# Optimization experiments

Hardware: AMD Instinct MI355X
Metric: run time of the kernel (lower is better)

Reference implementation:

```python
import jax, jax.numpy as jnp
import numpy as np

EMBED = 1024
HEADS = 16
HEAD_DIM = EMBED // HEADS
SCALING = HEAD_DIM ** -0.5
R = 16
LORA_SCALE = 32.0 / R  # alpha / r
NEG = jnp.finfo(jnp.float32).min


def lora_linear(x, W, A, B):
    # y = x @ W.T + (x @ A.T) @ B.T * scale   (LinearLora, bias=False)
    return x @ W.T + ((x @ A.T) @ B.T) * LORA_SCALE


def setup_inputs() -> dict:
    key = jax.random.key(0)
    ks = jax.random.split(key, 14)
    B, T, D = 1, 4096, EMBED
    hidden_states = jax.random.normal(ks[0], (B, T, D), jnp.float32)
    # causal additive mask (bsz, 1, tgt, src): 0 on/below diag, dtype-min above
    i = jnp.arange(T)
    causal = jnp.where(i[:, None] >= i[None, :], 0.0, NEG).astype(jnp.float32)
    attention_mask = jnp.broadcast_to(causal, (B, 1, T, T))
    s = 0.02
    def w(k, shape):
        return jax.random.normal(k, shape, jnp.float32) * s
    return dict(
        hidden_states=hidden_states,
        attention_mask=attention_mask,
        Wq=w(ks[1], (D, D)), Wk=w(ks[2], (D, D)), Wv=w(ks[3], (D, D)), Wo=w(ks[4], (D, D)),
        Aq=w(ks[5], (R, D)), Bq=jnp.zeros((D, R), jnp.float32) + w(ks[6], (D, R)),
        Ak=w(ks[7], (R, D)), Bk=w(ks[8], (D, R)),
        Av=w(ks[9], (R, D)), Bv=w(ks[10], (D, R)),
        Ao=w(ks[11], (R, D)), Bo=w(ks[12], (D, R)),
    )


def reference(hidden_states, attention_mask, Wq, Wk, Wv, Wo,
              Aq, Bq, Ak, Bk, Av, Bv, Ao, Bo):
    bsz, tgt_len, _ = hidden_states.shape
    H, Hd = HEADS, HEAD_DIM

    q = lora_linear(hidden_states, Wq, Aq, Bq) * SCALING
    k = lora_linear(hidden_states, Wk, Ak, Bk)
    v = lora_linear(hidden_states, Wv, Av, Bv)

    # (b, t, H, Hd)
    q = q.reshape(bsz, tgt_len, H, Hd)
    k = k.reshape(bsz, tgt_len, H, Hd)
    v = v.reshape(bsz, tgt_len, H, Hd)

    # scores (b, H, t, s)
    attn = jnp.einsum('bthd,bshd->bhts', q, k)
    attn = attn + attention_mask
    attn = jnp.maximum(attn, NEG)
    attn = jax.nn.softmax(attn, axis=-1)  # dropout p=0 / eval mode

    out = jnp.einsum('bhts,bshd->bthd', attn, v)
    out = out.reshape(bsz, tgt_len, H * Hd)
    out = lora_linear(out, Wo, Ao, Bo)
    return out
```

## Files before the change

kernel.cpp:

```cpp
#include <hip/hip_runtime.h>
#include <cmath>
#include <cstdint>

typedef unsigned short u16;
typedef __attribute__((ext_vector_type(8))) __bf16 bf16x8;
typedef __attribute__((ext_vector_type(4))) __bf16 bf16x4;
typedef __attribute__((ext_vector_type(4))) short s16x4;
typedef __attribute__((ext_vector_type(4))) float f32x4;

__device__ __forceinline__ u16 f2bf(float f) {
    union { float f; unsigned u; } v; v.f = f;
    unsigned r = v.u + 0x7fffu + ((v.u >> 16) & 1u);
    return (u16)(r >> 16);
}

__device__ __forceinline__ void gload_lds(const u16* g, u16* l) {
    __builtin_amdgcn_global_load_lds((__attribute__((address_space(1))) void*)g,
                                     (__attribute__((address_space(3))) void*)l,
                                     16, 0, 0);
}

__device__ __forceinline__ f32x4 mfma16(s16x4 a, s16x4 b, f32x4 c) {
#if __has_builtin(__builtin_amdgcn_mfma_f32_16x16x16bf16_1k)
    return __builtin_amdgcn_mfma_f32_16x16x16bf16_1k(a, b, c, 0, 0, 0);
#else
    asm("v_mfma_f32_16x16x16_bf16 %0, %1, %2, %3"
        : "=v"(c) : "v"(a), "v"(b), "0"(c));
    return c;
#endif
}

__global__ __launch_bounds__(256) void prep_all(
        const float* __restrict__ X,
        const float* __restrict__ Wq, const float* __restrict__ Wk,
        const float* __restrict__ Wv, const float* __restrict__ Wo,
        const float* __restrict__ Aq, const float* __restrict__ Bq,
        const float* __restrict__ Ak, const float* __restrict__ Bk,
        const float* __restrict__ Av, const float* __restrict__ Bv,
        const float* __restrict__ Ao, const float* __restrict__ Bo,
        u16* __restrict__ Wqkv, u16* __restrict__ Wob, u16* __restrict__ Xb) {
    const int p = blockIdx.y;
    const int idx = blockIdx.x * 256 + threadIdx.x;
    if (p == 4) {
        float4 v = ((const float4*)X)[idx];
        ushort4 o;
        o.x = f2bf(v.x); o.y = f2bf(v.y); o.z = f2bf(v.z); o.w = f2bf(v.w);
        ((ushort4*)Xb)[idx] = o;
        return;
    }
    const int n = idx >> 10, d = idx & 1023;
    const float* W; const float* A; const float* B;
    switch (p) {
        case 0: W = Wq; A = Aq; B = Bq; break;
        case 1: W = Wk; A = Ak; B = Bk; break;
        case 2: W = Wv; A = Av; B = Bv; break;
        default: W = Wo; A = Ao; B = Bo; break;
    }
    float lora = 0.f;
#pragma unroll
    for (int r = 0; r < 16; r++) lora += B[n * 16 + r] * A[r * 1024 + d];
    float v = W[idx] + 2.0f * lora;
    if (p == 0) v *= 0.125f * 1.44269504088896340736f;
    if (p < 3) Wqkv[(size_t)p * 1048576 + idx] = f2bf(v);
    else       Wob[idx] = f2bf(v);
}

template <bool F32OUT>
__global__ __launch_bounds__(256, 3) void gemm_bt(const u16* __restrict__ A,
                                                  const u16* __restrict__ B,
                                                  void* __restrict__ C, int ldc) {
    __shared__ __align__(16) u16 As[128 * 64];
    __shared__ __align__(16) u16 Bs[128 * 64];
    const int tid = threadIdx.x;
    const int lane = tid & 63, wave = tid >> 6;
    const int quad = lane >> 4, l16 = lane & 15;
    const int wm = (wave >> 1) * 64, wn = (wave & 1) * 64;
    const size_t m0 = (size_t)blockIdx.y * 128, n0 = (size_t)blockIdx.x * 128;
    const u16* Ap = A + m0 * 1024;
    const u16* Bp = B + n0 * 1024;
    const int xsw = l16 & 7;
    f32x4 acc[4][4] = {};
    for (int k0 = 0; k0 < 1024; k0 += 64) {
#pragma unroll
        for (int hh = 0; hh < 4; hh++) {
            int c = tid + hh * 256;
            int row = c >> 3, cg = (c & 7) ^ (row & 7);
            gload_lds(Ap + (size_t)row * 1024 + k0 + cg * 8, As + c * 8);
            gload_lds(Bp + (size_t)row * 1024 + k0 + cg * 8, Bs + c * 8);
        }
        asm volatile("s_waitcnt vmcnt(0)" ::: "memory");
        __syncthreads();
#pragma unroll
        for (int kf = 0; kf < 2; kf++) {
            bf16x8 af[4], bfr[4];
#pragma unroll
            for (int i = 0; i < 4; i++) {
                af[i]  = *(const bf16x8*)(As + (wm + i * 16 + l16) * 64
                                             + ((kf * 4 + quad) ^ xsw) * 8);
                bfr[i] = *(const bf16x8*)(Bs + (wn + i * 16 + l16) * 64
                                             + ((kf * 4 + quad) ^ xsw) * 8);
            }
#pragma unroll
            for (int mi = 0; mi < 4; mi++)
#pragma unroll
                for (int ni = 0; ni < 4; ni++)
                    acc[mi][ni] = __builtin_amdgcn_mfma_f32_16x16x32_bf16(
                            af[mi], bfr[ni], acc[mi][ni], 0, 0, 0);
        }
        __syncthreads();
    }
#pragma unroll
    for (int mi = 0; mi < 4; mi++)
#pragma unroll
        for (int ni = 0; ni < 4; ni++)
#pragma unroll
            for (int r = 0; r < 4; r++) {
                size_t row = m0 + wm + mi * 16 + quad * 4 + r;
                size_t col = n0 + wn + ni * 16 + l16;
                if (F32OUT) ((float*)C)[row * ldc + col] = acc[mi][ni][r];
                else        ((u16*)C)[row * ldc + col] = f2bf(acc[mi][ni][r]);
            }
}

template <bool F32OUT>
__global__ __launch_bounds__(256, 3) void gemm_bt64(const u16* __restrict__ A,
                                                    const u16* __restrict__ B,
                                                    void* __restrict__ C, int ldc) {
    __shared__ __align__(16) u16 As[64 * 64];
    __shared__ __align__(16) u16 Bs[128 * 64];
    const int tid = threadIdx.x;
    const int lane = tid & 63, wave = tid >> 6;
    const int quad = lane >> 4, l16 = lane & 15;
    const int wm = (wave >> 1) * 32, wn = (wave & 1) * 64;
    const size_t m0 = (size_t)blockIdx.y * 64, n0 = (size_t)blockIdx.x * 128;
    const u16* Ap = A + m0 * 1024;
    const u16* Bp = B + n0 * 1024;
    const int xsw = l16 & 7;
    f32x4 acc[2][4] = {};
    for (int k0 = 0; k0 < 1024; k0 += 64) {
#pragma unroll
        for (int hh = 0; hh < 2; hh++) {
            int c = tid + hh * 256;
            int row = c >> 3, cg = (c & 7) ^ (row & 7);
            gload_lds(Ap + (size_t)row * 1024 + k0 + cg * 8, As + c * 8);
        }
#pragma unroll
        for (int hh = 0; hh < 4; hh++) {
            int c = tid + hh * 256;
            int row = c >> 3, cg = (c & 7) ^ (row & 7);
            gload_lds(Bp + (size_t)row * 1024 + k0 + cg * 8, Bs + c * 8);
        }
        asm volatile("s_waitcnt vmcnt(0)" ::: "memory");
        __syncthreads();
#pragma unroll
        for (int kf = 0; kf < 2; kf++) {
            bf16x8 af[2], bfr[4];
#pragma unroll
            for (int i = 0; i < 2; i++)
                af[i] = *(const bf16x8*)(As + (wm + i * 16 + l16) * 64
                                            + ((kf * 4 + quad) ^ xsw) * 8);
#pragma unroll
            for (int i = 0; i < 4; i++)
                bfr[i] = *(const bf16x8*)(Bs + (wn + i * 16 + l16) * 64
                                             + ((kf * 4 + quad) ^ xsw) * 8);
#pragma unroll
            for (int mi = 0; mi < 2; mi++)
#pragma unroll
                for (int ni = 0; ni < 4; ni++)
                    acc[mi][ni] = __builtin_amdgcn_mfma_f32_16x16x32_bf16(
                            af[mi], bfr[ni], acc[mi][ni], 0, 0, 0);
        }
        __syncthreads();
    }
#pragma unroll
    for (int mi = 0; mi < 2; mi++)
#pragma unroll
        for (int ni = 0; ni < 4; ni++)
#pragma unroll
            for (int r = 0; r < 4; r++) {
                size_t row = m0 + wm + mi * 16 + quad * 4 + r;
                size_t col = n0 + wn + ni * 16 + l16;
                if (F32OUT) ((float*)C)[row * ldc + col] = acc[mi][ni][r];
                else        ((u16*)C)[row * ldc + col] = f2bf(acc[mi][ni][r]);
            }
}

__global__ __launch_bounds__(256) void transpose_v(const u16* __restrict__ Y,
                                                   u16* __restrict__ Vt) {
    __shared__ u16 tile[64][68];
    const int dv0 = blockIdx.x * 64;
    const int t0  = blockIdx.y * 64;
    const int tid = threadIdx.x;
#pragma unroll
    for (int p = 0; p < 4; p++) {
        int pos = tid + p * 256;
        int row = pos >> 4;
        int c4  = (pos & 15) * 4;
        ushort4 v = *(const ushort4*)(Y + (size_t)(t0 + row) * 3072 + 2048 + dv0 + c4);
        tile[row][c4 + 0] = v.x; tile[row][c4 + 1] = v.y;
        tile[row][c4 + 2] = v.z; tile[row][c4 + 3] = v.w;
    }
    __syncthreads();
#pragma unroll
    for (int p = 0; p < 4; p++) {
        int pos = tid + p * 256;
        int orow = pos >> 4;
        int oc4  = (pos & 15) * 4;
        ushort4 o;
        o.x = tile[oc4 + 0][orow]; o.y = tile[oc4 + 1][orow];
        o.z = tile[oc4 + 2][orow]; o.w = tile[oc4 + 3][orow];
        *(ushort4*)(Vt + (size_t)(dv0 + orow) * 4096 + t0 + oc4) = o;
    }
}

__device__ const unsigned char SCHED[48] = {
    (1<<6)|31, (0<<6)|15, (1<<6)|30, (2<<6)|30, (2<<6)|29, (0<<6)|14, (2<<6)|28, (1<<6)|27,
    (2<<6)|27, (0<<6)|13, (2<<6)|26, (2<<6)|25, (0<<6)|12, (1<<6)|24, (2<<6)|24, (2<<6)|23,
    (2<<6)|31, (1<<6)|29, (1<<6)|28, (1<<6)|26, (1<<6)|25, (1<<6)|23, (1<<6)|22, (1<<6)|21,
    (1<<6)|20, (2<<6)|20, (1<<6)|19, (2<<6)|19, (2<<6)|21, (2<<6)|22, (0<<6)|10, (0<<6)|11,
    (0<<6)|0,  (0<<6)|1,  (0<<6)|2,  (0<<6)|3,  (0<<6)|4,  (0<<6)|5,  (0<<6)|6,  (0<<6)|7,
    (1<<6)|16, (2<<6)|16, (1<<6)|18, (0<<6)|9,  (1<<6)|17, (2<<6)|17, (2<<6)|18, (0<<6)|8
};

__global__ __launch_bounds__(256, 3) void flash_attn(
        const u16* __restrict__ Y,
        const u16* __restrict__ Vt,
        u16* __restrict__ O,
        float* __restrict__ OpA,
        float* __restrict__ OpB,
        float* __restrict__ lA,
        float* __restrict__ lB) {
    __shared__ __align__(16) u16 lds[16384];
    const int tid = threadIdx.x;
    const int wave = tid >> 6, lane = tid & 63;
    const int quad = lane >> 4, l16 = lane & 15;
    const int bid = blockIdx.x;
    const int g = bid >> 4, h = bid & 15;
    const int sc = SCHED[g];
    const int p = sc & 63, mode = sc >> 6;
    const int t0 = (mode == 2) ? p + 1 : 0;
    const int t1 = (mode == 1) ? p + 1 : 2 * p + 2;
    const int q0w = p * 128 + wave * 32;
    const u16* Kbase = Y + 1024 + h * 64;
    const u16* Vbase = Vt + (size_t)(h * 64) * 4096;
    const int xsw = l16 & 7;

    bf16x8 qf[2][2];
#pragma unroll
    for (int qh = 0; qh < 2; qh++)
#pragma unroll
        for (int kf = 0; kf < 2; kf++)
            qf[qh][kf] = *(const bf16x8*)(Y + (size_t)(q0w + qh * 16 + l16) * 3072
                                            + h * 64 + kf * 32 + quad * 8);

    f32x4 oaccT[2][4] = {};
    f32x4 lacc[2] = {};
    const s16x4 ones = { (short)0x3F80, (short)0x3F80,
                         (short)0x3F80, (short)0x3F80 };

    {
        const int s0p = t0 * 64;
        u16* Kn = lds + (t0 & 1) * 8192;
#pragma unroll
        for (int pp = 0; pp < 2; pp++) {
            int c = pp * 256 + tid;
            int row = c >> 3, cg = (c & 7) ^ (row & 7);
            gload_lds(Kbase + (size_t)(s0p + row) * 3072 + cg * 8, Kn + c * 8);
            gload_lds(Vbase + (size_t)row * 4096 + s0p + cg * 8, Kn + 4096 + c * 8);
        }
    }

#pragma unroll 1
    for (int t = t0; t < t1; t++) {
        const int s0 = t * 64;
        u16* Ks = lds + (t & 1) * 8192;
        u16* Vs = Ks + 4096;
        asm volatile("s_waitcnt vmcnt(0)" ::: "memory");
        __syncthreads();

        if (t + 1 < t1) {
            u16* Kn = lds + ((t + 1) & 1) * 8192;
            const int sn = s0 + 64;
#pragma unroll
            for (int pp = 0; pp < 2; pp++) {
                int c = pp * 256 + tid;
                int row = c >> 3, cg = (c & 7) ^ (row & 7);
                gload_lds(Kbase + (size_t)(sn + row) * 3072 + cg * 8, Kn + c * 8);
                gload_lds(Vbase + (size_t)row * 4096 + sn + cg * 8, Kn + 4096 + c * 8);
            }
        }

        bf16x8 kfr[4][2];
#pragma unroll
        for (int ni = 0; ni < 4; ni++) {
            int row = ni * 16 + l16;
            kfr[ni][0] = *(const bf16x8*)(Ks + row * 64 + ((quad) ^ xsw) * 8);
            kfr[ni][1] = *(const bf16x8*)(Ks + row * 64 + ((4 + quad) ^ xsw) * 8);
        }
        s16x4 vfr[4][4];
#pragma unroll
        for (int nj = 0; nj < 4; nj++) {
            int row = nj * 16 + l16;
#pragma unroll
            for (int ni = 0; ni < 4; ni++) {
                int cc = ni * 2 + (quad >> 1);
                vfr[nj][ni] = *(const s16x4*)(Vs + row * 64 + (cc ^ xsw) * 8
                                                 + (quad & 1) * 4);
            }
        }

        const bool diag = (t >= 2 * p);
#pragma unroll
        for (int qh = 0; qh < 2; qh++) {
            f32x4 sacc[4] = {};
#pragma unroll
            for (int ni = 0; ni < 4; ni++) {
                sacc[ni] = __builtin_amdgcn_mfma_f32_16x16x32_bf16(
                        kfr[ni][0], qf[qh][0], sacc[ni], 0, 0, 0);
                sacc[ni] = __builtin_amdgcn_mfma_f32_16x16x32_bf16(
                        kfr[ni][1], qf[qh][1], sacc[ni], 0, 0, 0);
            }
            const int qg = q0w + qh * 16 + l16;
#pragma unroll
            for (int ni = 0; ni < 4; ni++) {
                if (diag) {
#pragma unroll
                    for (int r = 0; r < 4; r++) {
                        int sg = s0 + ni * 16 + quad * 4 + r;
                        if (sg > qg) sacc[ni][r] = -INFINITY;
                    }
                }
                f32x4 pe;
#pragma unroll
                for (int r = 0; r < 4; r++)
                    pe[r] = __builtin_amdgcn_exp2f(sacc[ni][r]);
                bf16x4 tt = { (__bf16)pe[0], (__bf16)pe[1],
                              (__bf16)pe[2], (__bf16)pe[3] };
                s16x4 pf = __builtin_bit_cast(s16x4, tt);
                lacc[qh] = mfma16(ones, pf, lacc[qh]);
#pragma unroll
                for (int nj = 0; nj < 4; nj++)
                    oaccT[qh][nj] = mfma16(vfr[nj][ni], pf, oaccT[qh][nj]);
            }
        }
    }

    __syncthreads();
    if (mode == 0) {
        u16* scr = lds + wave * 1152;
#pragma unroll
        for (int qh = 0; qh < 2; qh++) {
            float inv = 1.0f / lacc[qh][0];
#pragma unroll
            for (int nj = 0; nj < 4; nj++) {
                bf16x4 t4 = { (__bf16)(oaccT[qh][nj][0] * inv),
                              (__bf16)(oaccT[qh][nj][1] * inv),
                              (__bf16)(oaccT[qh][nj][2] * inv),
                              (__bf16)(oaccT[qh][nj][3] * inv) };
                *(s16x4*)(scr + l16 * 72 + nj * 16 + quad * 4) =
                        __builtin_bit_cast(s16x4, t4);
            }
            asm volatile("s_waitcnt lgkmcnt(0)" ::: "memory");
#pragma unroll
            for (int pp = 0; pp < 2; pp++) {
                int row = pp * 8 + (lane >> 3);
                int seg = (lane & 7) * 8;
                bf16x8 d = *(const bf16x8*)(scr + row * 72 + seg);
                *(bf16x8*)(O + (size_t)(q0w + qh * 16 + row) * 1024 + h * 64 + seg) = d;
            }
            asm volatile("s_waitcnt lgkmcnt(0)" ::: "memory");
        }
    } else {
        float* Op = (mode == 1) ? OpA : OpB;
        float* lp = (mode == 1) ? lA : lB;
        float* scr = (float*)lds + wave * 1088;
#pragma unroll
        for (int qh = 0; qh < 2; qh++) {
#pragma unroll
            for (int nj = 0; nj < 4; nj++)
                *(f32x4*)(scr + l16 * 68 + nj * 16 + quad * 4) = oaccT[qh][nj];
            asm volatile("s_waitcnt lgkmcnt(0)" ::: "memory");
#pragma unroll
            for (int it = 0; it < 4; it++) {
                int row = (lane >> 4) + it * 4;
                int seg = (lane & 15) * 4;
                f32x4 d = *(const f32x4*)(scr + row * 68 + seg);
                *(f32x4*)(Op + (size_t)(q0w + qh * 16 + row - 2048) * 1024
                             + h * 64 + seg) = d;
            }
            if (lane < 16)
                lp[(size_t)(q0w + qh * 16 + lane - 2048) * 16 + h] = lacc[qh][0];
            asm volatile("s_waitcnt lgkmcnt(0)" ::: "memory");
        }
    }
}

__global__ __launch_bounds__(256) void combine_o(
        const float* __restrict__ OpA, const float* __restrict__ OpB,
        const float* __restrict__ lA, const float* __restrict__ lB,
        u16* __restrict__ O) {
    const int idx = blockIdx.x * 256 + threadIdx.x;
    const int r = idx >> 7;
    const int c8 = (idx & 127) * 8;
    const int h = c8 >> 6;
    const float inv = 1.0f / (lA[r * 16 + h] + lB[r * 16 + h]);
    const float* a = OpA + (size_t)r * 1024 + c8;
    const float* b = OpB + (size_t)r * 1024 + c8;
    float4 a0 = *(const float4*)a, a1 = *(const float4*)(a + 4);
    float4 b0 = *(const float4*)b, b1 = *(const float4*)(b + 4);
    ushort4 o0, o1;
    o0.x = f2bf((a0.x + b0.x) * inv); o0.y = f2bf((a0.y + b0.y) * inv);
    o0.z = f2bf((a0.z + b0.z) * inv); o0.w = f2bf((a0.w + b0.w) * inv);
    o1.x = f2bf((a1.x + b1.x) * inv); o1.y = f2bf((a1.y + b1.y) * inv);
    o1.z = f2bf((a1.z + b1.z) * inv); o1.w = f2bf((a1.w + b1.w) * inv);
    u16* op = O + (size_t)(2048 + r) * 1024 + c8;
    *(ushort4*)op = o0;
    *(ushort4*)(op + 4) = o1;
}


extern "C" void kernel_launch(void* const* d_in, const int* in_sizes, int n_in,
                              void* d_out, int out_size, void* d_ws, size_t ws_size,
                              hipStream_t stream) {
    const float* X  = (const float*)d_in[0];
    const float* Wq = (const float*)d_in[2];
    const float* Wk = (const float*)d_in[3];
    const float* Wv = (const float*)d_in[4];
    const float* Wo = (const float*)d_in[5];
    const float* Aq = (const float*)d_in[6];
    const float* Bq = (const float*)d_in[7];
    const float* Ak = (const float*)d_in[8];
    const float* Bk = (const float*)d_in[9];
    const float* Av = (const float*)d_in[10];
    const float* Bv = (const float*)d_in[11];
    const float* Ao = (const float*)d_in[12];
    const float* Bo = (const float*)d_in[13];

    char* ws = (char*)d_ws;
    u16*   Xb   = (u16*)(ws);
    float* OpA  = (float*)(ws);
    u16*   Wqkv = (u16*)(ws + (8u  << 20));
    float* OpB  = (float*)(ws + (8u  << 20));
    u16*   Y    = (u16*)(ws + (16u << 20));
    u16*   Vt   = (u16*)(ws + (40u << 20));
    u16*   Ob   = (u16*)(ws + (48u << 20));
    u16*   Wob  = (u16*)(ws + (56u << 20));
    float* lA   = (float*)(ws + (58u << 20));
    float* lB   = (float*)(ws + (58u << 20) + (128u << 10));

    prep_all<<<dim3(4096, 5), 256, 0, stream>>>(X, Wq, Wk, Wv, Wo, Aq, Bq, Ak, Bk,
                                                Av, Bv, Ao, Bo, Wqkv, Wob, Xb);
    gemm_bt<false><<<dim3(24, 32), 256, 0, stream>>>(Xb, Wqkv, Y, 3072);
    transpose_v<<<dim3(16, 64), 256, 0, stream>>>(Y, Vt);
    flash_attn<<<dim3(768), 256, 0, stream>>>(Y, Vt, Ob, OpA, OpB, lA, lB);
    combine_o<<<dim3(1024), 256, 0, stream>>>(OpA, OpB, lA, lB, Ob);
    gemm_bt64<true><<<dim3(8, 64), 256, 0, stream>>>(Ob, Wob, d_out, 1024);
}
```

Measured before the change: 259.4 us.

## Load K/V fragments directly from global memory instead of staging through LDS

Removes the double-buffered LDS staging of K and V tiles (global_load_lds plus barriers) and has each wave load its K and V MFMA fragments straight from global memory through per-row pointers. It also shrinks the shared allocation to just the epilogue scratch space. This drops the per-iteration __syncthreads and the LDS traffic, but each of the four waves now fetches the same K/V data on its own, with no prefetch of the next tile to hide latency.

```diff
diff --git a/kernel.cpp b/kernel.cpp
--- a/kernel.cpp
+++ b/kernel.cpp
@@ -230,7 +230,7 @@
         float* __restrict__ OpB,
         float* __restrict__ lA,
         float* __restrict__ lB) {
-    __shared__ __align__(16) u16 lds[16384];
+    __shared__ __align__(16) u16 lds[8704];
     const int tid = threadIdx.x;
     const int wave = tid >> 6, lane = tid & 63;
     const int quad = lane >> 4, l16 = lane & 15;
@@ -241,9 +241,6 @@
     const int t0 = (mode == 2) ? p + 1 : 0;
     const int t1 = (mode == 1) ? p + 1 : 2 * p + 2;
     const int q0w = p * 128 + wave * 32;
-    const u16* Kbase = Y + 1024 + h * 64;
-    const u16* Vbase = Vt + (size_t)(h * 64) * 4096;
-    const int xsw = l16 & 7;
 
     bf16x8 qf[2][2];
 #pragma unroll
@@ -252,62 +249,42 @@
         for (int kf = 0; kf < 2; kf++)
             qf[qh][kf] = *(const bf16x8*)(Y + (size_t)(q0w + qh * 16 + l16) * 3072
                                             + h * 64 + kf * 32 + quad * 8);
+
+    const u16* kp[4];
+    const u16* vp[4];
+#pragma unroll
+    for (int ni = 0; ni < 4; ni++)
+        kp[ni] = Y + 1024 + h * 64 + quad * 8
+                   + (size_t)(t0 * 64 + ni * 16 + l16) * 3072;
+#pragma unroll
+    for (int nj = 0; nj < 4; nj++)
+        vp[nj] = Vt + (size_t)(h * 64 + nj * 16 + l16) * 4096
+                    + t0 * 64 + quad * 4;
 
     f32x4 oaccT[2][4] = {};
     f32x4 lacc[2] = {};
     const s16x4 ones = { (short)0x3F80, (short)0x3F80,
                          (short)0x3F80, (short)0x3F80 };
 
-    {
-        const int s0p = t0 * 64;
-        u16* Kn = lds + (t0 & 1) * 8192;
-#pragma unroll
-        for (int pp = 0; pp < 2; pp++) {
-            int c = pp * 256 + tid;
-            int row = c >> 3, cg = (c & 7) ^ (row & 7);
-            gload_lds(Kbase + (size_t)(s0p + row) * 3072 + cg * 8, Kn + c * 8);
-            gload_lds(Vbase + (size_t)row * 4096 + s0p + cg * 8, Kn + 4096 + c * 8);
-        }
-    }
-
 #pragma unroll 1
     for (int t = t0; t < t1; t++) {
         const int s0 = t * 64;
-        u16* Ks = lds + (t & 1) * 8192;
-        u16* Vs = Ks + 4096;
-        asm volatile("s_waitcnt vmcnt(0)" ::: "memory");
-        __syncthreads();
-
-        if (t + 1 < t1) {
-            u16* Kn = lds + ((t + 1) & 1) * 8192;
-            const int sn = s0 + 64;
-#pragma unroll
-            for (int pp = 0; pp < 2; pp++) {
-                int c = pp * 256 + tid;
-                int row = c >> 3, cg = (c & 7) ^ (row & 7);
-                gload_lds(Kbase + (size_t)(sn + row) * 3072 + cg * 8, Kn + c * 8);
-                gload_lds(Vbase + (size_t)row * 4096 + sn + cg * 8, Kn + 4096 + c * 8);
-            }
-        }
-
         bf16x8 kfr[4][2];
 #pragma unroll
         for (int ni = 0; ni < 4; ni++) {
-            int row = ni * 16 + l16;
-            kfr[ni][0] = *(const bf16x8*)(Ks + row * 64 + ((quad) ^ xsw) * 8);
-            kfr[ni][1] = *(const bf16x8*)(Ks + row * 64 + ((4 + quad) ^ xsw) * 8);
+            kfr[ni][0] = *(const bf16x8*)(kp[ni]);
+            kfr[ni][1] = *(const bf16x8*)(kp[ni] + 32);
         }
         s16x4 vfr[4][4];
 #pragma unroll
-        for (int nj = 0; nj < 4; nj++) {
-            int row = nj * 16 + l16;
-#pragma unroll
-            for (int ni = 0; ni < 4; ni++) {
-                int cc = ni * 2 + (quad >> 1);
-                vfr[nj][ni] = *(const s16x4*)(Vs + row * 64 + (cc ^ xsw) * 8
-                                                 + (quad & 1) * 4);
-            }
-        }
+        for (int nj = 0; nj < 4; nj++)
+#pragma unroll
+            for (int ni = 0; ni < 4; ni++)
+                vfr[nj][ni] = *(const s16x4*)(vp[nj] + ni * 16);
+#pragma unroll
+        for (int ni = 0; ni < 4; ni++) kp[ni] += 64 * 3072;
+#pragma unroll
+        for (int nj = 0; nj < 4; nj++) vp[nj] += 64;
 
         const bool diag = (t >= 2 * p);
 #pragma unroll
@@ -345,7 +322,6 @@
         }
     }
 
-    __syncthreads();
     if (mode == 0) {
         u16* scr = lds + wave * 1152;
 #pragma unroll
```

After: 388.7 us. 1.5x slower.

## Use 256-row query tiles for the second half in causal flash attention

Applied to the files above, without the earlier changes.

Rewrites the attention work schedule so that query blocks past row 2048 use 256-row tiles (four 16-row groups per wave), split into two KV-range halves, while the first half keeps 128-row tiles processed whole. Each K/V tile loaded into LDS is reused across more query rows, and the grid shrinks from 768 to 512 blocks. Occupancy is lowered to 2 blocks per CU to fit the larger accumulators, and s_setprio is wrapped around the MFMA bursts to favour matrix issue. The risks are register pressure, lower occupancy and load imbalance across the new schedule.

```diff
diff --git a/kernel.cpp b/kernel.cpp
--- a/kernel.cpp
+++ b/kernel.cpp
@@ -213,16 +213,20 @@
     }
 }
 
-__device__ const unsigned char SCHED[48] = {
-    (1<<6)|31, (0<<6)|15, (1<<6)|30, (2<<6)|30, (2<<6)|29, (0<<6)|14, (2<<6)|28, (1<<6)|27,
-    (2<<6)|27, (0<<6)|13, (2<<6)|26, (2<<6)|25, (0<<6)|12, (1<<6)|24, (2<<6)|24, (2<<6)|23,
-    (2<<6)|31, (1<<6)|29, (1<<6)|28, (1<<6)|26, (1<<6)|25, (1<<6)|23, (1<<6)|22, (1<<6)|21,
-    (1<<6)|20, (2<<6)|20, (1<<6)|19, (2<<6)|19, (2<<6)|21, (2<<6)|22, (0<<6)|10, (0<<6)|11,
-    (0<<6)|0,  (0<<6)|1,  (0<<6)|2,  (0<<6)|3,  (0<<6)|4,  (0<<6)|5,  (0<<6)|6,  (0<<6)|7,
-    (1<<6)|16, (2<<6)|16, (1<<6)|18, (0<<6)|9,  (1<<6)|17, (2<<6)|17, (2<<6)|18, (0<<6)|8
+#define SE(qb7, four, t0, t1) ((unsigned)(qb7) | ((unsigned)(four) << 5) | \
+                               ((unsigned)(t0) << 6) | ((unsigned)(t1) << 13))
+__device__ const unsigned SCHED[32] = {
+    SE(16,1,0,18), SE(18,1,0,20), SE(20,1,0,22), SE(22,1,0,24),
+    SE(24,1,0,26), SE(26,1,0,28), SE(28,1,0,30), SE(30,1,0,32),
+    SE(0,0,0,2),   SE(2,0,0,6),   SE(4,0,0,10),  SE(6,0,0,14),
+    SE(8,0,0,18),  SE(10,0,0,22), SE(12,0,0,26), SE(14,0,0,30),
+    SE(16,1,18,36), SE(18,1,20,40), SE(20,1,22,44), SE(22,1,24,48),
+    SE(24,1,26,52), SE(26,1,28,56), SE(28,1,30,60), SE(30,1,32,64),
+    SE(1,0,0,4),   SE(3,0,0,8),   SE(5,0,0,12),  SE(7,0,0,16),
+    SE(9,0,0,20),  SE(11,0,0,24), SE(13,0,0,28), SE(15,0,0,32)
 };
 
-__global__ __launch_bounds__(256, 3) void flash_attn(
+__global__ __launch_bounds__(256, 2) void flash_attn(
         const u16* __restrict__ Y,
         const u16* __restrict__ Vt,
         u16* __restrict__ O,
@@ -236,25 +240,29 @@
     const int quad = lane >> 4, l16 = lane & 15;
     const int bid = blockIdx.x;
     const int g = bid >> 4, h = bid & 15;
-    const int sc = SCHED[g];
-    const int p = sc & 63, mode = sc >> 6;
-    const int t0 = (mode == 2) ? p + 1 : 0;
-    const int t1 = (mode == 1) ? p + 1 : 2 * p + 2;
-    const int q0w = p * 128 + wave * 32;
+    const unsigned sc = SCHED[g];
+    const int qbase = (sc & 31) << 7;
+    const int four  = (sc >> 5) & 1;
+    const int t0    = (sc >> 6) & 127;
+    const int t1    = (sc >> 13) & 127;
+    const int nqh   = four ? 4 : 2;
+    const int tdiag = (sc & 31) << 1;
+    const int q0w = qbase + wave * (16 * nqh);
     const u16* Kbase = Y + 1024 + h * 64;
     const u16* Vbase = Vt + (size_t)(h * 64) * 4096;
     const int xsw = l16 & 7;
 
-    bf16x8 qf[2][2];
-#pragma unroll
-    for (int qh = 0; qh < 2; qh++)
-#pragma unroll
-        for (int kf = 0; kf < 2; kf++)
-            qf[qh][kf] = *(const bf16x8*)(Y + (size_t)(q0w + qh * 16 + l16) * 3072
-                                            + h * 64 + kf * 32 + quad * 8);
-
-    f32x4 oaccT[2][4] = {};
-    f32x4 lacc[2] = {};
+    bf16x8 qf[4][2];
+#pragma unroll
+    for (int qh = 0; qh < 4; qh++)
+        if (qh < nqh)
+#pragma unroll
+            for (int kf = 0; kf < 2; kf++)
+                qf[qh][kf] = *(const bf16x8*)(Y + (size_t)(q0w + qh * 16 + l16) * 3072
+                                                + h * 64 + kf * 32 + quad * 8);
+
+    f32x4 oaccT[4][4] = {};
+    f32x4 lacc[4] = {};
     const s16x4 ones = { (short)0x3F80, (short)0x3F80,
                          (short)0x3F80, (short)0x3F80 };
 
@@ -309,88 +317,99 @@
             }
         }
 
-        const bool diag = (t >= 2 * p);
-#pragma unroll
-        for (int qh = 0; qh < 2; qh++) {
-            f32x4 sacc[4] = {};
-#pragma unroll
-            for (int ni = 0; ni < 4; ni++) {
-                sacc[ni] = __builtin_amdgcn_mfma_f32_16x16x32_bf16(
-                        kfr[ni][0], qf[qh][0], sacc[ni], 0, 0, 0);
-                sacc[ni] = __builtin_amdgcn_mfma_f32_16x16x32_bf16(
-                        kfr[ni][1], qf[qh][1], sacc[ni], 0, 0, 0);
-            }
-            const int qg = q0w + qh * 16 + l16;
-#pragma unroll
-            for (int ni = 0; ni < 4; ni++) {
-                if (diag) {
-#pragma unroll
-                    for (int r = 0; r < 4; r++) {
-                        int sg = s0 + ni * 16 + quad * 4 + r;
-                        if (sg > qg) sacc[ni][r] = -INFINITY;
+        const bool diag = (t >= tdiag);
+#pragma unroll
+        for (int qh = 0; qh < 4; qh++) {
+            if (qh < nqh) {
+                f32x4 sacc[4] = {};
+                __builtin_amdgcn_s_setprio(1);
+#pragma unroll
+                for (int ni = 0; ni < 4; ni++) {
+                    sacc[ni] = __builtin_amdgcn_mfma_f32_16x16x32_bf16(
+                            kfr[ni][0], qf[qh][0], sacc[ni], 0, 0, 0);
+                    sacc[ni] = __builtin_amdgcn_mfma_f32_16x16x32_bf16(
+                            kfr[ni][1], qf[qh][1], sacc[ni], 0, 0, 0);
+                }
+                __builtin_amdgcn_s_setprio(0);
+                const int qg = q0w + qh * 16 + l16;
+#pragma unroll
+                for (int ni = 0; ni < 4; ni++) {
+                    if (diag) {
+#pragma unroll
+                        for (int r = 0; r < 4; r++) {
+                            int sg = s0 + ni * 16 + quad * 4 + r;
+                            if (sg > qg) sacc[ni][r] = -INFINITY;
+                        }
                     }
+                    f32x4 pe;
+#pragma unroll
+                    for (int r = 0; r < 4; r++)
+                        pe[r] = __builtin_amdgcn_exp2f(sacc[ni][r]);
+                    bf16x4 tt = { (__bf16)pe[0], (__bf16)pe[1],
+                                  (__bf16)pe[2], (__bf16)pe[3] };
+                    s16x4 pf = __builtin_bit_cast(s16x4, tt);
+                    __builtin_amdgcn_s_setprio(1);
+                    lacc[qh] = mfma16(ones, pf, lacc[qh]);
+#pragma unroll
+                    for (int nj = 0; nj < 4; nj++)
+                        oaccT[qh][nj] = mfma16(vfr[nj][ni], pf, oaccT[qh][nj]);
+                    __builtin_amdgcn_s_setprio(0);
                 }
-                f32x4 pe;
-#pragma unroll
-                for (int r = 0; r < 4; r++)
-                    pe[r] = __builtin_amdgcn_exp2f(sacc[ni][r]);
-                bf16x4 tt = { (__bf16)pe[0], (__bf16)pe[1],
-                              (__bf16)pe[2], (__bf16)pe[3] };
-                s16x4 pf = __builtin_bit_cast(s16x4, tt);
-                lacc[qh] = mfma16(ones, pf, lacc[qh]);
+            }
+        }
+    }
+
+    __syncthreads();
+    if (qbase < 2048) {
+        u16* scr = lds + wave * 1152;
+#pragma unroll
+        for (int qh = 0; qh < 4; qh++) {
+            if (qh < nqh) {
+                float inv = 1.0f / lacc[qh][0];
+#pragma unroll
+                for (int nj = 0; nj < 4; nj++) {
+                    bf16x4 t4 = { (__bf16)(oaccT[qh][nj][0] * inv),
+                                  (__bf16)(oaccT[qh][nj][1] * inv),
+                                  (__bf16)(oaccT[qh][nj][2] * inv),
+                                  (__bf16)(oaccT[qh][nj][3] * inv) };
+                    *(s16x4*)(scr + l16 * 72 + nj * 16 + quad * 4) =
+                            __builtin_bit_cast(s16x4, t4);
+                }
+                asm volatile("s_waitcnt lgkmcnt(0)" ::: "memory");
+#pragma unroll
+                for (int pp = 0; pp < 2; pp++) {
+                    int row = pp * 8 + (lane >> 3);
+                    int seg = (lane & 7) * 8;
+                    bf16x8 d = *(const bf16x8*)(scr + row * 72 + seg);
+                    *(bf16x8*)(O + (size_t)(q0w + qh * 16 + row) * 1024
+                                 + h * 64 + seg) = d;
+                }
+                asm volatile("s_waitcnt lgkmcnt(0)" ::: "memory");
+            }
+        }
+    } else {
+        float* Op = (t0 == 0) ? OpA : OpB;
+        float* lp = (t0 == 0) ? lA : lB;
+        float* scr = (float*)lds + wave * 1088;
+#pragma unroll
+        for (int qh = 0; qh < 4; qh++) {
+            if (qh < nqh) {
 #pragma unroll
                 for (int nj = 0; nj < 4; nj++)
-                    oaccT[qh][nj] = mfma16(vfr[nj][ni], pf, oaccT[qh][nj]);
-            }
-        }
-    }
-
-    __syncthreads();
-    if (mode == 0) {
-        u16* scr = lds + wave * 1152;
-#pragma unroll
-        for (int qh = 0; qh < 2; qh++) {
-            float inv = 1.0f / lacc[qh][0];
-#pragma unroll
-            for (int nj = 0; nj < 4; nj++) {
-                bf16x4 t4 = { (__bf16)(oaccT[qh][nj][0] * inv),
-                              (__bf16)(oaccT[qh][nj][1] * inv),
-                              (__bf16)(oaccT[qh][nj][2] * inv),
-                              (__bf16)(oaccT[qh][nj][3] * inv) };
-                *(s16x4*)(scr + l16 * 72 + nj * 16 + quad * 4) =
-                        __builtin_bit_cast(s16x4, t4);
-            }
-            asm volatile("s_waitcnt lgkmcnt(0)" ::: "memory");
-#pragma unroll
-            for (int pp = 0; pp < 2; pp++) {
-                int row = pp * 8 + (lane >> 3);
-                int seg = (lane & 7) * 8;
-                bf16x8 d = *(const bf16x8*)(scr + row * 72 + seg);
-                *(bf16x8*)(O + (size_t)(q0w + qh * 16 + row) * 1024 + h * 64 + seg) = d;
-            }
-            asm volatile("s_waitcnt lgkmcnt(0)" ::: "memory");
-        }
-    } else {
-        float* Op = (mode == 1) ? OpA : OpB;
-        float* lp = (mode == 1) ? lA : lB;
-        float* scr = (float*)lds + wave * 1088;
-#pragma unroll
-        for (int qh = 0; qh < 2; qh++) {
-#pragma unroll
-            for (int nj = 0; nj < 4; nj++)
-                *(f32x4*)(scr + l16 * 68 + nj * 16 + quad * 4) = oaccT[qh][nj];
-            asm volatile("s_waitcnt lgkmcnt(0)" ::: "memory");
-#pragma unroll
-            for (int it = 0; it < 4; it++) {
-                int row = (lane >> 4) + it * 4;
-                int seg = (lane & 15) * 4;
-                f32x4 d = *(const f32x4*)(scr + row * 68 + seg);
-                *(f32x4*)(Op + (size_t)(q0w + qh * 16 + row - 2048) * 1024
-                             + h * 64 + seg) = d;
-            }
-            if (lane < 16)
-                lp[(size_t)(q0w + qh * 16 + lane - 2048) * 16 + h] = lacc[qh][0];
-            asm volatile("s_waitcnt lgkmcnt(0)" ::: "memory");
+                    *(f32x4*)(scr + l16 * 68 + nj * 16 + quad * 4) = oaccT[qh][nj];
+                asm volatile("s_waitcnt lgkmcnt(0)" ::: "memory");
+#pragma unroll
+                for (int it = 0; it < 4; it++) {
+                    int row = (lane >> 4) + it * 4;
+                    int seg = (lane & 15) * 4;
+                    f32x4 d = *(const f32x4*)(scr + row * 68 + seg);
+                    *(f32x4*)(Op + (size_t)(q0w + qh * 16 + row - 2048) * 1024
+                                 + h * 64 + seg) = d;
+                }
+                if (lane < 16)
+                    lp[(size_t)(q0w + qh * 16 + lane - 2048) * 16 + h] = lacc[qh][0];
+                asm volatile("s_waitcnt lgkmcnt(0)" ::: "memory");
+            }
         }
     }
 }
@@ -452,7 +471,7 @@
                                                 Av, Bv, Ao, Bo, Wqkv, Wob, Xb);
     gemm_bt<false><<<dim3(24, 32), 256, 0, stream>>>(Xb, Wqkv, Y, 3072);
     transpose_v<<<dim3(16, 64), 256, 0, stream>>>(Y, Vt);
-    flash_attn<<<dim3(768), 256, 0, stream>>>(Y, Vt, Ob, OpA, OpB, lA, lB);
+    flash_attn<<<dim3(512), 256, 0, stream>>>(Y, Vt, Ob, OpA, OpB, lA, lB);
     combine_o<<<dim3(1024), 256, 0, stream>>>(OpA, OpB, lA, lB, Ob);
     gemm_bt64<true><<<dim3(8, 64), 256, 0, stream>>>(Ob, Wob, d_out, 1024);
 }
```

New measurement: 289.6 us. 1.12x slower.

## Fuse V transpose into QKV GEMM epilogue and split-combine into output GEMM

Applied to the files above, without the earlier changes.

The QKV GEMM now writes the V portion directly as a transposed Vt through a swizzled LDS scratch, removing the separate transpose_v kernel. The output projection GEMM now merges the two split-KV partial outputs and normalises them while loading the A tile for the lower half rows, removing the combine_o kernel. This saves two launches and the round trips of Y-V and Ob through global memory. In exchange, the combine work is repeated for every column block of the output GEMM, and those A loads become synchronous register loads instead of async global-to-LDS copies.

```diff
diff --git a/kernel.cpp b/kernel.cpp
--- a/kernel.cpp
+++ b/kernel.cpp
@@ -65,12 +65,13 @@
     else       Wob[idx] = f2bf(v);
 }
 
-template <bool F32OUT>
-__global__ __launch_bounds__(256, 3) void gemm_bt(const u16* __restrict__ A,
-                                                  const u16* __restrict__ B,
-                                                  void* __restrict__ C, int ldc) {
-    __shared__ __align__(16) u16 As[128 * 64];
-    __shared__ __align__(16) u16 Bs[128 * 64];
+__global__ __launch_bounds__(256, 3) void gemm_qkv(const u16* __restrict__ A,
+                                                   const u16* __restrict__ B,
+                                                   u16* __restrict__ Y,
+                                                   u16* __restrict__ Vt) {
+    __shared__ __align__(16) u16 AsBs[2 * 128 * 64];
+    u16* As = AsBs;
+    u16* Bs = AsBs + 8192;
     const int tid = threadIdx.x;
     const int lane = tid & 63, wave = tid >> 6;
     const int quad = lane >> 4, l16 = lane & 15;
@@ -109,23 +110,47 @@
         }
         __syncthreads();
     }
-#pragma unroll
-    for (int mi = 0; mi < 4; mi++)
-#pragma unroll
-        for (int ni = 0; ni < 4; ni++)
-#pragma unroll
-            for (int r = 0; r < 4; r++) {
-                size_t row = m0 + wm + mi * 16 + quad * 4 + r;
-                size_t col = n0 + wn + ni * 16 + l16;
-                if (F32OUT) ((float*)C)[row * ldc + col] = acc[mi][ni][r];
-                else        ((u16*)C)[row * ldc + col] = f2bf(acc[mi][ni][r]);
-            }
-}
-
-template <bool F32OUT>
-__global__ __launch_bounds__(256, 3) void gemm_bt64(const u16* __restrict__ A,
-                                                    const u16* __restrict__ B,
-                                                    void* __restrict__ C, int ldc) {
+    if (n0 < 2048) {
+#pragma unroll
+        for (int mi = 0; mi < 4; mi++)
+#pragma unroll
+            for (int ni = 0; ni < 4; ni++)
+#pragma unroll
+                for (int r = 0; r < 4; r++) {
+                    size_t row = m0 + wm + mi * 16 + quad * 4 + r;
+                    size_t col = n0 + wn + ni * 16 + l16;
+                    Y[row * 3072 + col] = f2bf(acc[mi][ni][r]);
+                }
+    } else {
+        __syncthreads();
+        u16* scr = AsBs + wave * 4096;
+#pragma unroll
+        for (int mi = 0; mi < 4; mi++)
+#pragma unroll
+            for (int ni = 0; ni < 4; ni++) {
+                int col = ni * 16 + l16;
+                int tb = (mi * 16 + quad * 4) ^ ((col & 7) << 3);
+                bf16x4 t4 = { (__bf16)acc[mi][ni][0], (__bf16)acc[mi][ni][1],
+                              (__bf16)acc[mi][ni][2], (__bf16)acc[mi][ni][3] };
+                *(s16x4*)(scr + col * 64 + tb) = __builtin_bit_cast(s16x4, t4);
+            }
+        asm volatile("s_waitcnt lgkmcnt(0)" ::: "memory");
+#pragma unroll
+        for (int pp = 0; pp < 8; pp++) {
+            int dv = pp * 8 + (lane >> 3);
+            int t8 = (lane & 7) * 8;
+            bf16x8 d = *(const bf16x8*)(scr + dv * 64 + (t8 ^ ((dv & 7) << 3)));
+            *(bf16x8*)(Vt + (size_t)(n0 - 2048 + wn + dv) * 4096
+                          + m0 + wm + t8) = d;
+        }
+    }
+}
+
+__global__ __launch_bounds__(256, 3) void gemm_out(
+        const u16* __restrict__ Ob, const u16* __restrict__ Wob,
+        const float* __restrict__ OpA, const float* __restrict__ OpB,
+        const float* __restrict__ lA, const float* __restrict__ lB,
+        float* __restrict__ C) {
     __shared__ __align__(16) u16 As[64 * 64];
     __shared__ __align__(16) u16 Bs[128 * 64];
     const int tid = threadIdx.x;
@@ -133,16 +158,39 @@
     const int quad = lane >> 4, l16 = lane & 15;
     const int wm = (wave >> 1) * 32, wn = (wave & 1) * 64;
     const size_t m0 = (size_t)blockIdx.y * 64, n0 = (size_t)blockIdx.x * 128;
-    const u16* Ap = A + m0 * 1024;
-    const u16* Bp = B + n0 * 1024;
+    const u16* Ap = Ob + m0 * 1024;
+    const u16* Bp = Wob + n0 * 1024;
     const int xsw = l16 & 7;
+    const bool part = (m0 >= 2048);
     f32x4 acc[2][4] = {};
     for (int k0 = 0; k0 < 1024; k0 += 64) {
-#pragma unroll
-        for (int hh = 0; hh < 2; hh++) {
-            int c = tid + hh * 256;
-            int row = c >> 3, cg = (c & 7) ^ (row & 7);
-            gload_lds(Ap + (size_t)row * 1024 + k0 + cg * 8, As + c * 8);
+        if (!part) {
+#pragma unroll
+            for (int hh = 0; hh < 2; hh++) {
+                int c = tid + hh * 256;
+                int row = c >> 3, cg = (c & 7) ^ (row & 7);
+                gload_lds(Ap + (size_t)row * 1024 + k0 + cg * 8, As + c * 8);
+            }
+        } else {
+            const int h = k0 >> 6;
+#pragma unroll
+            for (int hh = 0; hh < 2; hh++) {
+                int c = tid + hh * 256;
+                int row = c >> 3, cg = (c & 7) ^ (row & 7);
+                int rr = (int)m0 + row - 2048;
+                const float* pa = OpA + (size_t)rr * 1024 + k0 + cg * 8;
+                const float* pb = OpB + (size_t)rr * 1024 + k0 + cg * 8;
+                float inv = 1.0f / (lA[rr * 16 + h] + lB[rr * 16 + h]);
+                float4 a0 = *(const float4*)pa, a1 = *(const float4*)(pa + 4);
+                float4 b0 = *(const float4*)pb, b1 = *(const float4*)(pb + 4);
+                ushort4 o0, o1;
+                o0.x = f2bf((a0.x + b0.x) * inv); o0.y = f2bf((a0.y + b0.y) * inv);
+                o0.z = f2bf((a0.z + b0.z) * inv); o0.w = f2bf((a0.w + b0.w) * inv);
+                o1.x = f2bf((a1.x + b1.x) * inv); o1.y = f2bf((a1.y + b1.y) * inv);
+                o1.z = f2bf((a1.z + b1.z) * inv); o1.w = f2bf((a1.w + b1.w) * inv);
+                *(ushort4*)(As + c * 8) = o0;
+                *(ushort4*)(As + c * 8 + 4) = o1;
+            }
         }
 #pragma unroll
         for (int hh = 0; hh < 4; hh++) {
@@ -180,37 +228,8 @@
             for (int r = 0; r < 4; r++) {
                 size_t row = m0 + wm + mi * 16 + quad * 4 + r;
                 size_t col = n0 + wn + ni * 16 + l16;
-                if (F32OUT) ((float*)C)[row * ldc + col] = acc[mi][ni][r];
-                else        ((u16*)C)[row * ldc + col] = f2bf(acc[mi][ni][r]);
-            }
-}
-
-__global__ __launch_bounds__(256) void transpose_v(const u16* __restrict__ Y,
-                                                   u16* __restrict__ Vt) {
-    __shared__ u16 tile[64][68];
-    const int dv0 = blockIdx.x * 64;
-    const int t0  = blockIdx.y * 64;
-    const int tid = threadIdx.x;
-#pragma unroll
-    for (int p = 0; p < 4; p++) {
-        int pos = tid + p * 256;
-        int row = pos >> 4;
-        int c4  = (pos & 15) * 4;
-        ushort4 v = *(const ushort4*)(Y + (size_t)(t0 + row) * 3072 + 2048 + dv0 + c4);
-        tile[row][c4 + 0] = v.x; tile[row][c4 + 1] = v.y;
-        tile[row][c4 + 2] = v.z; tile[row][c4 + 3] = v.w;
-    }
-    __syncthreads();
-#pragma unroll
-    for (int p = 0; p < 4; p++) {
-        int pos = tid + p * 256;
-        int orow = pos >> 4;
-        int oc4  = (pos & 15) * 4;
-        ushort4 o;
-        o.x = tile[oc4 + 0][orow]; o.y = tile[oc4 + 1][orow];
-        o.z = tile[oc4 + 2][orow]; o.w = tile[oc4 + 3][orow];
-        *(ushort4*)(Vt + (size_t)(dv0 + orow) * 4096 + t0 + oc4) = o;
-    }
+                C[row * 1024 + col] = acc[mi][ni][r];
+            }
 }
 
 __device__ const unsigned char SCHED[48] = {
@@ -395,29 +414,6 @@
     }
 }
 
-__global__ __launch_bounds__(256) void combine_o(
-        const float* __restrict__ OpA, const float* __restrict__ OpB,
-        const float* __restrict__ lA, const float* __restrict__ lB,
-        u16* __restrict__ O) {
-    const int idx = blockIdx.x * 256 + threadIdx.x;
-    const int r = idx >> 7;
-    const int c8 = (idx & 127) * 8;
-    const int h = c8 >> 6;
-    const float inv = 1.0f / (lA[r * 16 + h] + lB[r * 16 + h]);
-    const float* a = OpA + (size_t)r * 1024 + c8;
-    const float* b = OpB + (size_t)r * 1024 + c8;
-    float4 a0 = *(const float4*)a, a1 = *(const float4*)(a + 4);
-    float4 b0 = *(const float4*)b, b1 = *(const float4*)(b + 4);
-    ushort4 o0, o1;
-    o0.x = f2bf((a0.x + b0.x) * inv); o0.y = f2bf((a0.y + b0.y) * inv);
-    o0.z = f2bf((a0.z + b0.z) * inv); o0.w = f2bf((a0.w + b0.w) * inv);
-    o1.x = f2bf((a1.x + b1.x) * inv); o1.y = f2bf((a1.y + b1.y) * inv);
-    o1.z = f2bf((a1.z + b1.z) * inv); o1.w = f2bf((a1.w + b1.w) * inv);
-    u16* op = O + (size_t)(2048 + r) * 1024 + c8;
-    *(ushort4*)op = o0;
-    *(ushort4*)(op + 4) = o1;
-}
-
 
 extern "C" void kernel_launch(void* const* d_in, const int* in_sizes, int n_in,
                               void* d_out, int out_size, void* d_ws, size_t ws_size,
@@ -450,9 +446,8 @@
 
     prep_all<<<dim3(4096, 5), 256, 0, stream>>>(X, Wq, Wk, Wv, Wo, Aq, Bq, Ak, Bk,
                                                 Av, Bv, Ao, Bo, Wqkv, Wob, Xb);
-    gemm_bt<false><<<dim3(24, 32), 256, 0, stream>>>(Xb, Wqkv, Y, 3072);
-    transpose_v<<<dim3(16, 64), 256, 0, stream>>>(Y, Vt);
+    gemm_qkv<<<dim3(24, 32), 256, 0, stream>>>(Xb, Wqkv, Y, Vt);
     flash_attn<<<dim3(768), 256, 0, stream>>>(Y, Vt, Ob, OpA, OpB, lA, lB);
-    combine_o<<<dim3(1024), 256, 0, stream>>>(OpA, OpB, lA, lB, Ob);
-    gemm_bt64<true><<<dim3(8, 64), 256, 0, stream>>>(Ob, Wob, d_out, 1024);
-}
+    gemm_out<<<dim3(8, 64), 256, 0, stream>>>(Ob, Wob, OpA, OpB, lA, lB,
+                                              (float*)d_out);
+}
```

Result: no change. 261.9 us (+1.0%).
